# Performance work log

Measured on AMD Instinct MI355X. Metric: run time of the kernel, lower is better.

## Reference

```python
import jax, jax.numpy as jnp
import numpy as np

B, S, D, H, K = 8, 4096, 1024, 16, 256
DH = D // H  # attention_head_size = 64


def setup_inputs() -> dict:
    key = jax.random.key(0)
    ks = jax.random.split(key, 12)
    hidden_states = jax.random.normal(ks[0], (B, S, D), dtype=jnp.float32)
    # ragged lengths in [S/2, S]; HF-style additive mask: 0 valid, -10000 pad
    lengths = jax.random.randint(ks[1], (B,), S // 2, S + 1)
    attention_mask = jnp.where(
        jnp.arange(S)[None, :] < lengths[:, None], 0.0, -10000.0
    ).astype(jnp.float32)[:, None, None, :]  # [B,1,1,S]
    std = 0.02
    Wq = jax.random.normal(ks[2], (D, D), dtype=jnp.float32) * std
    bq = jnp.zeros((D,), dtype=jnp.float32)
    Wk = jax.random.normal(ks[3], (D, D), dtype=jnp.float32) * std
    bk = jnp.zeros((D,), dtype=jnp.float32)
    Wv = jax.random.normal(ks[4], (D, D), dtype=jnp.float32) * std
    bv = jnp.zeros((D,), dtype=jnp.float32)
    # nn.init.normal_(std=1.0), shape [max_position_embeddings, k]
    proj_k = jax.random.normal(ks[5], (S, K), dtype=jnp.float32)
    proj_v = jax.random.normal(ks[6], (S, K), dtype=jnp.float32)
    return dict(hidden_states=hidden_states, attention_mask=attention_mask,
                Wq=Wq, bq=bq, Wk=Wk, bk=bk, Wv=Wv, bv=bv,
                proj_k=proj_k, proj_v=proj_v)


def reference(hidden_states, attention_mask, Wq, bq, Wk, bk, Wv, bv, proj_k, proj_v):
    Bn, Sn, Dn = hidden_states.shape
    dt = hidden_states.dtype
    # lengths[i] = number of valid tokens (mask entries > -1)
    lengths = jnp.sum(attention_mask[:, 0, 0, :] > -1, axis=-1)  # [B] int
    m = (jnp.arange(Sn)[None, :] < lengths[:, None]).astype(dt)  # [B,S] valid mask
    pk = proj_k[:Sn]  # [S,K]
    pv = proj_v[:Sn]
    hk = hidden_states @ Wk.T + bk  # [B,S,D]
    hv = hidden_states @ Wv.T + bv
    # ragged projection: per sample, proj[:L_i]^T @ h[i,:L_i] / sqrt(L_i)
    # vectorized as a masked contraction (zeros beyond L_i contribute nothing)
    inv_sqrt_len = 1.0 / jnp.sqrt(lengths.astype(dt))  # [B]
    hkp = jnp.einsum('bs,sk,bsd->bkd', m, pk, hk) * inv_sqrt_len[:, None, None]
    hvp = jnp.einsum('bs,sk,bsd->bkd', m, pv, hv) * inv_sqrt_len[:, None, None]
    # split heads: [B,*,H,DH] -> [B,H,*,DH]
    q = (hidden_states @ Wq.T + bq).reshape(Bn, Sn, H, DH).transpose(0, 2, 1, 3)
    k = hkp.reshape(Bn, K, H, DH).transpose(0, 2, 1, 3)
    v = hvp.reshape(Bn, K, H, DH).transpose(0, 2, 1, 3)
    scores = jnp.einsum('bhsd,bhkd->bhsk', q, k) / np.float32(np.sqrt(DH))
    probs = jax.nn.softmax(scores, axis=-1)  # dropout p=0 (eval) -> identity
    ctx = jnp.einsum('bhsk,bhkd->bhsd', probs, v)
    return ctx.transpose(0, 2, 1, 3).reshape(Bn, Sn, Dn)
```

## Files before the change

kernel.cpp:

```cpp
#include <hip/hip_runtime.h>
#include <stdint.h>

#define B_ 8
#define S_ 4096
#define D_ 1024
#define H_ 16
#define K_ 256
#define DH_ 64

typedef unsigned short ushort_t;
typedef __attribute__((ext_vector_type(8))) short short8;
typedef __attribute__((ext_vector_type(4))) short short4x;
typedef __attribute__((ext_vector_type(4))) float floatx4;

static __device__ __forceinline__ float u2f(unsigned short u){
  union { float f; unsigned int i; } v; v.i = ((unsigned int)u) << 16; return v.f;
}
static __device__ __forceinline__ unsigned short f2u(float f){
  union { float f; unsigned int i; } v; v.f = f;
  unsigned int r = v.i + 0x7fffu + ((v.i >> 16) & 1u);
  return (unsigned short)(r >> 16);
}

__global__ __launch_bounds__(256) void k_len(const float* __restrict__ mask,
                                             int* __restrict__ len, float* __restrict__ invl){
  int b = blockIdx.x, t = threadIdx.x;
  __shared__ int cnt[256];
  int c = 0;
  for(int s = t; s < S_; s += 256) c += (mask[b*S_ + s] > -1.0f) ? 1 : 0;
  cnt[t] = c; __syncthreads();
  for(int o = 128; o > 0; o >>= 1){ if(t < o) cnt[t] += cnt[t+o]; __syncthreads(); }
  if(t == 0){ len[b] = cnt[0]; invl[b] = rsqrtf((float)cnt[0]); }
}

__global__ __launch_bounds__(256) void k_sp_part(const float* __restrict__ pk, const float* __restrict__ pv,
                                                 const float* __restrict__ mask, float* __restrict__ part){
  int c = blockIdx.x;
  int b = blockIdx.y;
  int sel = blockIdx.z;
  const float* p = sel ? pv : pk;
  int k = threadIdx.x;
  int s0 = c * 128;
  float acc = 0.f;
  for(int i = 0; i < 128; i++){
    int s = s0 + i;
    float mm = mask[b*S_ + s];
    if(mm > -1.0f) acc += p[(size_t)s*K_ + k];
  }
  part[(((size_t)(b*2 + sel))*32 + c)*K_ + k] = acc;
}

__global__ __launch_bounds__(256) void k_sp_red(const float* __restrict__ part, const float* __restrict__ invl,
                                                float* __restrict__ spk, float* __restrict__ spv){
  int b = blockIdx.x, sel = blockIdx.y, k = threadIdx.x;
  float acc = 0.f;
#pragma unroll
  for(int c = 0; c < 32; c++) acc += part[(((size_t)(b*2 + sel))*32 + c)*K_ + k];
  float r = acc * invl[b];
  if(sel) spv[b*K_ + k] = r; else spk[b*K_ + k] = r;
}

__global__ __launch_bounds__(256) void k_cvt(const float* __restrict__ src, ushort_t* __restrict__ dst, int n4){
  int i = blockIdx.x * 256 + threadIdx.x;
  if(i >= n4) return;
  const float4 a = *(const float4*)(src + i*4);
  short4x v;
  v[0] = (short)f2u(a.x); v[1] = (short)f2u(a.y); v[2] = (short)f2u(a.z); v[3] = (short)f2u(a.w);
  *(short4x*)(dst + i*4) = v;
}

__global__ __launch_bounds__(256) void k_trcvt(const float* __restrict__ src, ushort_t* __restrict__ dst,
                                               int R, int C, long sstride, long dstride){
  __shared__ __align__(16) short t[64*66];
  const float* s0 = src + (size_t)blockIdx.z * sstride;
  ushort_t* d0 = dst + (size_t)blockIdx.z * dstride;
  int r0 = blockIdx.y * 64, c0 = blockIdx.x * 64;
  int tid = threadIdx.x;
#pragma unroll
  for(int i = 0; i < 2; i++){
    int f = tid + 256*i;
    int r = f >> 3, c = (f & 7) * 8;
    const float* p = s0 + (size_t)(r0 + r) * C + (c0 + c);
    float4 a = *(const float4*)p;
    float4 b2 = *(const float4*)(p + 4);
    short* q = &t[r*66 + c];
    q[0]=(short)f2u(a.x); q[1]=(short)f2u(a.y); q[2]=(short)f2u(a.z); q[3]=(short)f2u(a.w);
    q[4]=(short)f2u(b2.x); q[5]=(short)f2u(b2.y); q[6]=(short)f2u(b2.z); q[7]=(short)f2u(b2.w);
  }
  __syncthreads();
#pragma unroll
  for(int i = 0; i < 2; i++){
    int f = tid + 256*i;
    int dc = f >> 3, sg = f & 7;
    short8 v;
#pragma unroll
    for(int j = 0; j < 8; j++) v[j] = t[(sg*8 + j)*66 + dc];
    *(short8*)(d0 + (size_t)(c0 + dc) * R + (r0 + sg*8)) = v;
  }
}

__global__ __launch_bounds__(256) void k_xp(const ushort_t* __restrict__ pkT, const ushort_t* __restrict__ pvT,
      const ushort_t* __restrict__ XT, const int* __restrict__ len, const float* __restrict__ invl,
      ushort_t* __restrict__ XpK, ushort_t* __restrict__ XpV){
  int b = blockIdx.y, sel = blockIdx.z;
  const ushort_t* A = sel ? pvT : pkT;
  ushort_t* hi = sel ? XpV : XpK;
  int m0 = (blockIdx.x & 1) * 128;
  int n0 = (blockIdx.x >> 1) * 128;
  const ushort_t* Bm = XT + (size_t)b * D_ * S_;
  int L = len[b];
  int nk = (L + 31) >> 5;
  bool tail = (L & 31) != 0;
  __shared__ __align__(16) short As[128*32];
  __shared__ __align__(16) short Bs[128*32];
  int tid = threadIdx.x, lane = tid & 63, w = tid >> 6;
  int mW = (w & 1) * 64, nW = (w >> 1) * 64;
  int lm = lane & 15, lk = (lane >> 4) * 8;
  floatx4 acc[4][4];
#pragma unroll
  for(int i = 0; i < 4; i++)
#pragma unroll
    for(int j = 0; j < 4; j++) acc[i][j] = (floatx4)0.f;
  for(int ks = 0; ks < nk; ks++){
    int k0 = ks << 5;
    short8 va[2], vb[2];
#pragma unroll
    for(int i = 0; i < 2; i++){
      int f = i*256 + tid;
      int row = f >> 2, col = (f & 3) * 8;
      va[i] = *(const short8*)(A  + (size_t)(m0+row)*S_ + (k0+col));
      vb[i] = *(const short8*)(Bm + (size_t)(n0+row)*S_ + (k0+col));
    }
    if(tail && ks == nk-1){
      int rlim = L - k0;
#pragma unroll
      for(int i = 0; i < 2; i++){
        int col = ((i*256 + tid) & 3) * 8;
#pragma unroll
        for(int j = 0; j < 8; j++) if(col + j >= rlim) va[i][j] = 0;
      }
    }
    __syncthreads();
#pragma unroll
    for(int i = 0; i < 2; i++){
      int f = i*256 + tid;
      *(short8*)&As[f*8] = va[i];
      *(short8*)&Bs[f*8] = vb[i];
    }
    __syncthreads();
    short8 af[4], bfr[4];
#pragma unroll
    for(int i = 0; i < 4; i++) af[i]  = *(const short8*)&As[(mW + 16*i + lm)*32 + lk];
#pragma unroll
    for(int j = 0; j < 4; j++) bfr[j] = *(const short8*)&Bs[(nW + 16*j + lm)*32 + lk];
#pragma unroll
    for(int i = 0; i < 4; i++)
#pragma unroll
      for(int j = 0; j < 4; j++)
        acc[i][j] = __builtin_amdgcn_mfma_f32_16x16x32_bf16(af[i], bfr[j], acc[i][j], 0, 0, 0);
  }
  float sc = invl[b];
#pragma unroll
  for(int i = 0; i < 4; i++){
#pragma unroll
    for(int j = 0; j < 4; j++){
      int col = n0 + nW + 16*j + lm;
#pragma unroll
      for(int r = 0; r < 4; r++){
        int row = m0 + mW + 16*i + (lane>>4)*4 + r;
        hi[((size_t)b*K_ + row)*D_ + col] = f2u(acc[i][j][r] * sc);
      }
    }
  }
}

__global__ __launch_bounds__(256) void k_kv(const ushort_t* __restrict__ XpK, const ushort_t* __restrict__ XpV,
      const ushort_t* __restrict__ Wk, const ushort_t* __restrict__ Wv,
      const float* __restrict__ bk, const float* __restrict__ bv,
      const float* __restrict__ spk, const float* __restrict__ spv,
      ushort_t* __restrict__ kten, ushort_t* __restrict__ vTt){
  int b = blockIdx.y, sel = blockIdx.z;
  const ushort_t* Ab = (sel ? XpV : XpK) + (size_t)b*K_*D_;
  const ushort_t* W = sel ? Wv : Wk;
  const float* bias = sel ? bv : bk;
  const float* sp = (sel ? spv : spk) + b*K_;
  int m0 = (blockIdx.x & 1) * 128;
  int n0 = (blockIdx.x >> 1) * 128;
  __shared__ __align__(16) short As[128*32];
  __shared__ __align__(16) short Bs[128*32];
  int tid = threadIdx.x, lane = tid & 63, w = tid >> 6;
  int mW = (w & 1) * 64, nW = (w >> 1) * 64;
  int lm = lane & 15, lk = (lane >> 4) * 8;
  floatx4 acc[4][4];
#pragma unroll
  for(int i = 0; i < 4; i++)
#pragma unroll
    for(int j = 0; j < 4; j++) acc[i][j] = (floatx4)0.f;
  for(int ks = 0; ks < 32; ks++){
    int k0 = ks << 5;
    short8 va[2], vb[2];
#pragma unroll
    for(int i = 0; i < 2; i++){
      int f = i*256 + tid;
      int row = f >> 2, col = (f & 3) * 8;
      va[i] = *(const short8*)(Ab + (size_t)(m0+row)*D_ + (k0+col));
      vb[i] = *(const short8*)(W  + (size_t)(n0+row)*D_ + (k0+col));
    }
    __syncthreads();
#pragma unroll
    for(int i = 0; i < 2; i++){
      int f = i*256 + tid;
      *(short8*)&As[f*8] = va[i];
      *(short8*)&Bs[f*8] = vb[i];
    }
    __syncthreads();
    short8 af[4], bfr[4];
#pragma unroll
    for(int i = 0; i < 4; i++) af[i]  = *(const short8*)&As[(mW + 16*i + lm)*32 + lk];
#pragma unroll
    for(int j = 0; j < 4; j++) bfr[j] = *(const short8*)&Bs[(nW + 16*j + lm)*32 + lk];
#pragma unroll
    for(int i = 0; i < 4; i++)
#pragma unroll
      for(int j = 0; j < 4; j++)
        acc[i][j] = __builtin_amdgcn_mfma_f32_16x16x32_bf16(af[i], bfr[j], acc[i][j], 0, 0, 0);
  }
#pragma unroll
  for(int j = 0; j < 4; j++){
    int col = n0 + nW + 16*j + lm;
    float bb = bias[col];
    int hcol = col >> 6, dcol = col & 63;
#pragma unroll
    for(int i = 0; i < 4; i++){
#pragma unroll
      for(int r = 0; r < 4; r++){
        int row = m0 + mW + 16*i + (lane>>4)*4 + r;
        float val = acc[i][j][r] + sp[row]*bb;
        if(sel == 0) kten[(((size_t)b*H_ + hcol)*K_ + row)*DH_ + dcol] = f2u(val);
        else         vTt [(((size_t)b*H_ + hcol)*DH_ + dcol)*K_ + row] = f2u(val);
      }
    }
  }
}

__global__ __launch_bounds__(256) void k_q(const float* __restrict__ X, const ushort_t* __restrict__ Wq,
                                           const float* __restrict__ bq, float* __restrict__ out){
  int m0 = (int)(blockIdx.x >> 3) * 128;
  int n0 = (int)(blockIdx.x & 7) * 128;
  __shared__ __align__(16) short As[128*32];
  __shared__ __align__(16) short Bs[128*32];
  int tid = threadIdx.x, lane = tid & 63, w = tid >> 6;
  int mW = (w & 1) * 64, nW = (w >> 1) * 64;
  int lm = lane & 15, lk = (lane >> 4) * 8;
  floatx4 acc[4][4];
#pragma unroll
  for(int i = 0; i < 4; i++)
#pragma unroll
    for(int j = 0; j < 4; j++) acc[i][j] = (floatx4)0.f;
  for(int ks = 0; ks < 32; ks++){
    int k0 = ks << 5;
    short8 va[2], vb[2];
#pragma unroll
    for(int i = 0; i < 2; i++){
      int f = i*256 + tid;
      int row = f >> 2, col = (f & 3) * 8;
      const float* p = X + (size_t)(m0+row)*D_ + (k0+col);
      float4 a = *(const float4*)p;
      float4 b2 = *(const float4*)(p + 4);
      short8 v;
      v[0]=(short)f2u(a.x); v[1]=(short)f2u(a.y); v[2]=(short)f2u(a.z); v[3]=(short)f2u(a.w);
      v[4]=(short)f2u(b2.x); v[5]=(short)f2u(b2.y); v[6]=(short)f2u(b2.z); v[7]=(short)f2u(b2.w);
      va[i] = v;
      vb[i] = *(const short8*)(Wq + (size_t)(n0+row)*D_ + (k0+col));
    }
    __syncthreads();
#pragma unroll
    for(int i = 0; i < 2; i++){
      int f = i*256 + tid;
      *(short8*)&As[f*8] = va[i];
      *(short8*)&Bs[f*8] = vb[i];
    }
    __syncthreads();
    short8 af[4], bfr[4];
#pragma unroll
    for(int i = 0; i < 4; i++) af[i]  = *(const short8*)&As[(mW + 16*i + lm)*32 + lk];
#pragma unroll
    for(int j = 0; j < 4; j++) bfr[j] = *(const short8*)&Bs[(nW + 16*j + lm)*32 + lk];
#pragma unroll
    for(int i = 0; i < 4; i++)
#pragma unroll
      for(int j = 0; j < 4; j++)
        acc[i][j] = __builtin_amdgcn_mfma_f32_16x16x32_bf16(af[i], bfr[j], acc[i][j], 0, 0, 0);
  }
#pragma unroll
  for(int j = 0; j < 4; j++){
    int col = n0 + nW + 16*j + lm;
    float bb = bq[col];
#pragma unroll
    for(int i = 0; i < 4; i++){
#pragma unroll
      for(int r = 0; r < 4; r++){
        int row = m0 + mW + 16*i + (lane>>4)*4 + r;
        out[(size_t)row*D_ + col] = acc[i][j][r] + bb;
      }
    }
  }
}

__global__ __launch_bounds__(256) void k_attn(float* __restrict__ out,
                                              const ushort_t* __restrict__ kten,
                                              const ushort_t* __restrict__ vTt){
  int x = blockIdx.x;
  int h = x & 15, b = (x >> 4) & 7, st = x >> 7;
  int s0 = st * 64;
  __shared__ __align__(16) short q_s[8*64*8];
  __shared__ __align__(16) short kp_s[8*256*8];
  __shared__ __align__(16) short v_s[32*64*8];
  int tid = threadIdx.x, lane = tid & 63, w = tid >> 6;
  int lm = lane & 15, lq = lane >> 4;
  const ushort_t* kb_g = kten + ((size_t)b*H_ + h)*K_*DH_;
  const ushort_t* vb_g = vTt + ((size_t)b*H_ + h)*DH_*K_;
  const float* qb_g = out + ((size_t)b*S_ + s0)*D_ + h*DH_;
  short8 vq[2], vk[8], vv[8];
#pragma unroll
  for(int i = 0; i < 2; i++){
    int f = i*256 + tid;
    const float* p = qb_g + (size_t)(f & 63)*D_ + (f >> 6)*8;
    float4 a = *(const float4*)p;
    float4 b2 = *(const float4*)(p + 4);
    short8 v;
    v[0]=(short)f2u(a.x); v[1]=(short)f2u(a.y); v[2]=(short)f2u(a.z); v[3]=(short)f2u(a.w);
    v[4]=(short)f2u(b2.x); v[5]=(short)f2u(b2.y); v[6]=(short)f2u(b2.z); v[7]=(short)f2u(b2.w);
    vq[i] = v;
  }
#pragma unroll
  for(int i = 0; i < 8; i++){
    int f = i*256 + tid;
    vk[i] = *(const short8*)(kb_g + (f & 255)*DH_ + (f >> 8)*8);
  }
#pragma unroll
  for(int i = 0; i < 8; i++){
    int f = i*256 + tid;
    vv[i] = *(const short8*)(vb_g + (f & 63)*K_ + (f >> 6)*8);
  }
#pragma unroll
  for(int i = 0; i < 2; i++) *(short8*)&q_s[(i*256 + tid)*8] = vq[i];
#pragma unroll
  for(int i = 0; i < 8; i++) *(short8*)&kp_s[(i*256 + tid)*8] = vk[i];
#pragma unroll
  for(int i = 0; i < 8; i++) *(short8*)&v_s[(i*256 + tid)*8] = vv[i];
  __syncthreads();

  int rw = w * 16;
  floatx4 accS[16];
#pragma unroll
  for(int n = 0; n < 16; n++) accS[n] = (floatx4)0.f;
#pragma unroll
  for(int ks = 0; ks < 2; ks++){
    int kb = ks*4 + lq;
    short8 a = *(const short8*)&q_s[(kb*64 + rw + lm)*8];
#pragma unroll
    for(int n = 0; n < 16; n++){
      short8 bf_ = *(const short8*)&kp_s[(kb*256 + 16*n + lm)*8];
      accS[n] = __builtin_amdgcn_mfma_f32_16x16x32_bf16(a, bf_, accS[n], 0, 0, 0);
    }
  }
  const float scl = 0.125f;
  float invr[4];
#pragma unroll
  for(int r = 0; r < 4; r++){
    float mx = -1e30f;
#pragma unroll
    for(int n = 0; n < 16; n++) mx = fmaxf(mx, accS[n][r]);
    mx = fmaxf(mx, __shfl_xor(mx, 1));
    mx = fmaxf(mx, __shfl_xor(mx, 2));
    mx = fmaxf(mx, __shfl_xor(mx, 4));
    mx = fmaxf(mx, __shfl_xor(mx, 8));
    float sum = 0.f;
#pragma unroll
    for(int n = 0; n < 16; n++){
      float p = __expf((accS[n][r] - mx) * scl);
      accS[n][r] = p;
      sum += p;
    }
    sum += __shfl_xor(sum, 1);
    sum += __shfl_xor(sum, 2);
    sum += __shfl_xor(sum, 4);
    sum += __shfl_xor(sum, 8);
    invr[r] = 1.f / sum;
  }
  __syncthreads();
  short* p_s = &kp_s[w * 4096];
#pragma unroll
  for(int n = 0; n < 16; n++){
    int kb2 = 2*n + (lm >> 3);
    int e = lane & 7;
#pragma unroll
    for(int r = 0; r < 4; r++){
      int row = lq*4 + r;
      p_s[(kb2*16 + row)*8 + e] = (short)f2u(accS[n][r]);
    }
  }
  floatx4 accC[4];
#pragma unroll
  for(int n = 0; n < 4; n++) accC[n] = (floatx4)0.f;
#pragma unroll
  for(int ks = 0; ks < 8; ks++){
    int kb = ks*4 + lq;
    short8 a = *(const short8*)&p_s[(kb*16 + lm)*8];
#pragma unroll
    for(int n = 0; n < 4; n++){
      short8 bf_ = *(const short8*)&v_s[(kb*64 + 16*n + lm)*8];
      accC[n] = __builtin_amdgcn_mfma_f32_16x16x32_bf16(a, bf_, accC[n], 0, 0, 0);
    }
  }
#pragma unroll
  for(int n = 0; n < 4; n++){
#pragma unroll
    for(int r = 0; r < 4; r++){
      int srow = s0 + rw + lq*4 + r;
      out[((size_t)b*S_ + srow)*D_ + h*DH_ + 16*n + lm] = accC[n][r] * invr[r];
    }
  }
}

extern "C" void kernel_launch(void* const* d_in, const int* in_sizes, int n_in,
                              void* d_out, int out_size, void* d_ws, size_t ws_size,
                              hipStream_t stream) {
  (void)in_sizes; (void)n_in; (void)out_size; (void)ws_size;
  const float* X    = (const float*)d_in[0];
  const float* mask = (const float*)d_in[1];
  const float* Wq   = (const float*)d_in[2];
  const float* bq   = (const float*)d_in[3];
  const float* Wk   = (const float*)d_in[4];
  const float* bk   = (const float*)d_in[5];
  const float* Wv   = (const float*)d_in[6];
  const float* bv   = (const float*)d_in[7];
  const float* pk   = (const float*)d_in[8];
  const float* pv   = (const float*)d_in[9];
  float* out = (float*)d_out;

  char* wsp = (char*)d_ws;
  int*   len  = (int*)wsp;
  float* invl = (float*)(wsp + 64);
  float* spk  = (float*)(wsp + 256);
  float* spv  = (float*)(wsp + 256 + 8192);
  ushort_t* pkT  = (ushort_t*)(wsp + 32768);
  ushort_t* pvT  = pkT  + (size_t)K_*S_;
  ushort_t* Wqb  = pvT  + (size_t)K_*S_;
  ushort_t* Wkb  = Wqb  + (size_t)D_*D_;
  ushort_t* Wvb  = Wkb  + (size_t)D_*D_;
  ushort_t* XpK  = Wvb  + (size_t)D_*D_;
  ushort_t* XpV  = XpK  + (size_t)B_*K_*D_;
  ushort_t* kten = XpV  + (size_t)B_*K_*D_;
  ushort_t* vTt  = kten + (size_t)B_*K_*D_;
  float* part = (float*)((char*)d_out + 100u*1024*1024);

  hipLaunchKernelGGL(k_len, dim3(8), dim3(256), 0, stream, mask, len, invl);
  hipLaunchKernelGGL(k_sp_part, dim3(32,8,2), dim3(256), 0, stream, pk, pv, mask, part);
  hipLaunchKernelGGL(k_sp_red,  dim3(8,2), dim3(256), 0, stream, part, invl, spk, spv);
  hipLaunchKernelGGL(k_cvt, dim3(1024), dim3(256), 0, stream, Wq, Wqb, D_*D_/4);
  hipLaunchKernelGGL(k_cvt, dim3(1024), dim3(256), 0, stream, Wk, Wkb, D_*D_/4);
  hipLaunchKernelGGL(k_cvt, dim3(1024), dim3(256), 0, stream, Wv, Wvb, D_*D_/4);
  hipLaunchKernelGGL(k_trcvt, dim3(4,64,1), dim3(256), 0, stream, pk, pkT, S_, K_, 0L, 0L);
  hipLaunchKernelGGL(k_trcvt, dim3(4,64,1), dim3(256), 0, stream, pv, pvT, S_, K_, 0L, 0L);
  hipLaunchKernelGGL(k_trcvt, dim3(16,64,8), dim3(256), 0, stream, X, (ushort_t*)out, S_, D_, (long)S_*D_, (long)D_*S_);
  hipLaunchKernelGGL(k_xp,  dim3(16,8,2), dim3(256), 0, stream, pkT, pvT, (const ushort_t*)out, len, invl, XpK, XpV);
  hipLaunchKernelGGL(k_kv,  dim3(16,8,2), dim3(256), 0, stream, XpK, XpV, Wkb, Wvb, bk, bv, spk, spv, kten, vTt);
  hipLaunchKernelGGL(k_q,   dim3(2048), dim3(256), 0, stream, X, Wqb, bq, out);
  hipLaunchKernelGGL(k_attn, dim3(8192), dim3(256), 0, stream, out, kten, vTt);
}
```

Before: 705.9 us.

## Emit bf16 copy of X alongside transpose; run Q GEMM and attention on bf16

The transpose-convert kernel now also writes a row-major bf16 copy of X into workspace. A new Q GEMM reads this bf16 X instead of converting fp32 on the fly, and it writes Q as bf16 to a workspace buffer rather than fp32 into the output. The attention kernel then loads bf16 Q, which halves Q traffic. The new path runs only when the workspace is large enough, so it needs about 128MB of extra scratch and falls back to the old path otherwise.

Measured after the change: 680.6 us. -3.6%, faster.

```diff
diff --git a/kernel.cpp b/kernel.cpp
--- a/kernel.cpp
+++ b/kernel.cpp
@@ -35,9 +35,7 @@
 
 __global__ __launch_bounds__(256) void k_sp_part(const float* __restrict__ pk, const float* __restrict__ pv,
                                                  const float* __restrict__ mask, float* __restrict__ part){
-  int c = blockIdx.x;
-  int b = blockIdx.y;
-  int sel = blockIdx.z;
+  int c = blockIdx.x, b = blockIdx.y, sel = blockIdx.z;
   const float* p = sel ? pv : pk;
   int k = threadIdx.x;
   int s0 = c * 128;
@@ -96,6 +94,44 @@
 #pragma unroll
     for(int j = 0; j < 8; j++) v[j] = t[(sg*8 + j)*66 + dc];
     *(short8*)(d0 + (size_t)(c0 + dc) * R + (r0 + sg*8)) = v;
+  }
+}
+
+__global__ __launch_bounds__(256) void k_trcvt_dual(const float* __restrict__ src, ushort_t* __restrict__ dstT,
+                                                    ushort_t* __restrict__ dstS, int R, int C,
+                                                    long sstride, long dTstride, long dSstride){
+  __shared__ __align__(16) short t[64*66];
+  const float* s0 = src + (size_t)blockIdx.z * sstride;
+  ushort_t* dT = dstT + (size_t)blockIdx.z * dTstride;
+  ushort_t* dS = dstS + (size_t)blockIdx.z * dSstride;
+  int r0 = blockIdx.y * 64, c0 = blockIdx.x * 64;
+  int tid = threadIdx.x;
+#pragma unroll
+  for(int i = 0; i < 2; i++){
+    int f = tid + 256*i;
+    int r = f >> 3, c = (f & 7) * 8;
+    const float* p = s0 + (size_t)(r0 + r) * C + (c0 + c);
+    float4 a = *(const float4*)p;
+    float4 b2 = *(const float4*)(p + 4);
+    short8 v;
+    v[0]=(short)f2u(a.x); v[1]=(short)f2u(a.y); v[2]=(short)f2u(a.z); v[3]=(short)f2u(a.w);
+    v[4]=(short)f2u(b2.x); v[5]=(short)f2u(b2.y); v[6]=(short)f2u(b2.z); v[7]=(short)f2u(b2.w);
+    *(short8*)(dS + (size_t)(r0 + r) * C + (c0 + c)) = v;
+    short* q = &t[r*66 + c];
+    const int* v32 = (const int*)&v;
+    int* q32 = (int*)q;
+#pragma unroll
+    for(int k2 = 0; k2 < 4; k2++) q32[k2] = v32[k2];
+  }
+  __syncthreads();
+#pragma unroll
+  for(int i = 0; i < 2; i++){
+    int f = tid + 256*i;
+    int dc = f >> 3, sg = f & 7;
+    short8 v;
+#pragma unroll
+    for(int j = 0; j < 8; j++) v[j] = t[(sg*8 + j)*66 + dc];
+    *(short8*)(dT + (size_t)(c0 + dc) * R + (r0 + sg*8)) = v;
   }
 }
 
@@ -307,6 +343,64 @@
   }
 }
 
+__global__ __launch_bounds__(256) void k_q2(const ushort_t* __restrict__ Xb, const ushort_t* __restrict__ Wq,
+                                            const float* __restrict__ bq, ushort_t* __restrict__ qb){
+  int m0 = (int)(blockIdx.x >> 3) * 128;
+  int n0 = (int)(blockIdx.x & 7) * 128;
+  __shared__ __align__(16) short As[128*32];
+  __shared__ __align__(16) short Bs[128*32];
+  int tid = threadIdx.x, lane = tid & 63, w = tid >> 6;
+  int mW = (w & 1) * 64, nW = (w >> 1) * 64;
+  int lm = lane & 15, lk = (lane >> 4) * 8;
+  floatx4 acc[4][4];
+#pragma unroll
+  for(int i = 0; i < 4; i++)
+#pragma unroll
+    for(int j = 0; j < 4; j++) acc[i][j] = (floatx4)0.f;
+  for(int ks = 0; ks < 32; ks++){
+    int k0 = ks << 5;
+    short8 va[2], vb[2];
+#pragma unroll
+    for(int i = 0; i < 2; i++){
+      int f = i*256 + tid;
+      int row = f >> 2, col = (f & 3) * 8;
+      va[i] = *(const short8*)(Xb + (size_t)(m0+row)*D_ + (k0+col));
+      vb[i] = *(const short8*)(Wq + (size_t)(n0+row)*D_ + (k0+col));
+    }
+    __syncthreads();
+#pragma unroll
+    for(int i = 0; i < 2; i++){
+      int f = i*256 + tid;
+      *(short8*)&As[f*8] = va[i];
+      *(short8*)&Bs[f*8] = vb[i];
+    }
+    __syncthreads();
+    short8 af[4], bfr[4];
+#pragma unroll
+    for(int i = 0; i < 4; i++) af[i]  = *(const short8*)&As[(mW + 16*i + lm)*32 + lk];
+#pragma unroll
+    for(int j = 0; j < 4; j++) bfr[j] = *(const short8*)&Bs[(nW + 16*j + lm)*32 + lk];
+#pragma unroll
+    for(int i = 0; i < 4; i++)
+#pragma unroll
+      for(int j = 0; j < 4; j++)
+        acc[i][j] = __builtin_amdgcn_mfma_f32_16x16x32_bf16(af[i], bfr[j], acc[i][j], 0, 0, 0);
+  }
+#pragma unroll
+  for(int j = 0; j < 4; j++){
+    int col = n0 + nW + 16*j + lm;
+    float bb = bq[col];
+#pragma unroll
+    for(int i = 0; i < 4; i++){
+#pragma unroll
+      for(int r = 0; r < 4; r++){
+        int row = m0 + mW + 16*i + (lane>>4)*4 + r;
+        qb[(size_t)row*D_ + col] = f2u(acc[i][j][r] + bb);
+      }
+    }
+  }
+}
+
 __global__ __launch_bounds__(256) void k_attn(float* __restrict__ out,
                                               const ushort_t* __restrict__ kten,
                                               const ushort_t* __restrict__ vTt){
@@ -424,10 +518,121 @@
   }
 }
 
+__global__ __launch_bounds__(256) void k_attn2(float* __restrict__ out, const ushort_t* __restrict__ qb,
+                                               const ushort_t* __restrict__ kten,
+                                               const ushort_t* __restrict__ vTt){
+  int x = blockIdx.x;
+  int h = x & 15, b = (x >> 4) & 7, st = x >> 7;
+  int s0 = st * 64;
+  __shared__ __align__(16) short q_s[8*64*8];
+  __shared__ __align__(16) short kp_s[8*256*8];
+  __shared__ __align__(16) short v_s[32*64*8];
+  int tid = threadIdx.x, lane = tid & 63, w = tid >> 6;
+  int lm = lane & 15, lq = lane >> 4;
+  const ushort_t* kb_g = kten + ((size_t)b*H_ + h)*K_*DH_;
+  const ushort_t* vb_g = vTt + ((size_t)b*H_ + h)*DH_*K_;
+  const ushort_t* qg = qb + ((size_t)b*S_ + s0)*D_ + h*DH_;
+  short8 vq[2], vk[8], vv[8];
+#pragma unroll
+  for(int i = 0; i < 2; i++){
+    int f = i*256 + tid;
+    vq[i] = *(const short8*)(qg + (size_t)(f & 63)*D_ + (f >> 6)*8);
+  }
+#pragma unroll
+  for(int i = 0; i < 8; i++){
+    int f = i*256 + tid;
+    vk[i] = *(const short8*)(kb_g + (f & 255)*DH_ + (f >> 8)*8);
+  }
+#pragma unroll
+  for(int i = 0; i < 8; i++){
+    int f = i*256 + tid;
+    vv[i] = *(const short8*)(vb_g + (f & 63)*K_ + (f >> 6)*8);
+  }
+#pragma unroll
+  for(int i = 0; i < 2; i++) *(short8*)&q_s[(i*256 + tid)*8] = vq[i];
+#pragma unroll
+  for(int i = 0; i < 8; i++) *(short8*)&kp_s[(i*256 + tid)*8] = vk[i];
+#pragma unroll
+  for(int i = 0; i < 8; i++) *(short8*)&v_s[(i*256 + tid)*8] = vv[i];
+  __syncthreads();
+
+  int rw = w * 16;
+  floatx4 accS[16];
+#pragma unroll
+  for(int n = 0; n < 16; n++) accS[n] = (floatx4)0.f;
+#pragma unroll
+  for(int ks = 0; ks < 2; ks++){
+    int kb = ks*4 + lq;
+    short8 a = *(const short8*)&q_s[(kb*64 + rw + lm)*8];
+#pragma unroll
+    for(int n = 0; n < 16; n++){
+      short8 bf_ = *(const short8*)&kp_s[(kb*256 + 16*n + lm)*8];
+      accS[n] = __builtin_amdgcn_mfma_f32_16x16x32_bf16(a, bf_, accS[n], 0, 0, 0);
+    }
+  }
+  const float scl = 0.125f;
+  float invr[4];
+#pragma unroll
+  for(int r = 0; r < 4; r++){
+    float mx = -1e30f;
+#pragma unroll
+    for(int n = 0; n < 16; n++) mx = fmaxf(mx, accS[n][r]);
+    mx = fmaxf(mx, __shfl_xor(mx, 1));
+    mx = fmaxf(mx, __shfl_xor(mx, 2));
+    mx = fmaxf(mx, __shfl_xor(mx, 4));
+    mx = fmaxf(mx, __shfl_xor(mx, 8));
+    float sum = 0.f;
+#pragma unroll
+    for(int n = 0; n < 16; n++){
+      float p = __expf((accS[n][r] - mx) * scl);
+      accS[n][r] = p;
+      sum += p;
+    }
+    sum += __shfl_xor(sum, 1);
+    sum += __shfl_xor(sum, 2);
+    sum += __shfl_xor(sum, 4);
+    sum += __shfl_xor(sum, 8);
+    invr[r] = 1.f / sum;
+  }
+  __syncthreads();
+  short* p_s = &kp_s[w * 4096];
+#pragma unroll
+  for(int n = 0; n < 16; n++){
+    int kb2 = 2*n + (lm >> 3);
+    int e = lane & 7;
+#pragma unroll
+    for(int r = 0; r < 4; r++){
+      int row = lq*4 + r;
+      p_s[(kb2*16 + row)*8 + e] = (short)f2u(accS[n][r]);
+    }
+  }
+  floatx4 accC[4];
+#pragma unroll
+  for(int n = 0; n < 4; n++) accC[n] = (floatx4)0.f;
+#pragma unroll
+  for(int ks = 0; ks < 8; ks++){
+    int kb = ks*4 + lq;
+    short8 a = *(const short8*)&p_s[(kb*16 + lm)*8];
+#pragma unroll
+    for(int n = 0; n < 4; n++){
+      short8 bf_ = *(const short8*)&v_s[(kb*64 + 16*n + lm)*8];
+      accC[n] = __builtin_amdgcn_mfma_f32_16x16x32_bf16(a, bf_, accC[n], 0, 0, 0);
+    }
+  }
+#pragma unroll
+  for(int n = 0; n < 4; n++){
+#pragma unroll
+    for(int r = 0; r < 4; r++){
+      int srow = s0 + rw + lq*4 + r;
+      out[((size_t)b*S_ + srow)*D_ + h*DH_ + 16*n + lm] = accC[n][r] * invr[r];
+    }
+  }
+}
+
 extern "C" void kernel_launch(void* const* d_in, const int* in_sizes, int n_in,
                               void* d_out, int out_size, void* d_ws, size_t ws_size,
                               hipStream_t stream) {
-  (void)in_sizes; (void)n_in; (void)out_size; (void)ws_size;
+  (void)in_sizes; (void)n_in; (void)out_size;
   const float* X    = (const float*)d_in[0];
   const float* mask = (const float*)d_in[1];
   const float* Wq   = (const float*)d_in[2];
@@ -454,6 +659,10 @@
   ushort_t* XpV  = XpK  + (size_t)B_*K_*D_;
   ushort_t* kten = XpV  + (size_t)B_*K_*D_;
   ushort_t* vTt  = kten + (size_t)B_*K_*D_;
+  ushort_t* Xb   = vTt  + (size_t)B_*K_*D_;
+  ushort_t* qb   = Xb   + (size_t)B_*S_*D_;
+  size_t tier2_need = (size_t)((char*)(qb + (size_t)B_*S_*D_) - wsp);
+  int tier2 = ws_size >= tier2_need;
   float* part = (float*)((char*)d_out + 100u*1024*1024);
 
   hipLaunchKernelGGL(k_len, dim3(8), dim3(256), 0, stream, mask, len, invl);
@@ -464,9 +673,18 @@
   hipLaunchKernelGGL(k_cvt, dim3(1024), dim3(256), 0, stream, Wv, Wvb, D_*D_/4);
   hipLaunchKernelGGL(k_trcvt, dim3(4,64,1), dim3(256), 0, stream, pk, pkT, S_, K_, 0L, 0L);
   hipLaunchKernelGGL(k_trcvt, dim3(4,64,1), dim3(256), 0, stream, pv, pvT, S_, K_, 0L, 0L);
-  hipLaunchKernelGGL(k_trcvt, dim3(16,64,8), dim3(256), 0, stream, X, (ushort_t*)out, S_, D_, (long)S_*D_, (long)D_*S_);
-  hipLaunchKernelGGL(k_xp,  dim3(16,8,2), dim3(256), 0, stream, pkT, pvT, (const ushort_t*)out, len, invl, XpK, XpV);
-  hipLaunchKernelGGL(k_kv,  dim3(16,8,2), dim3(256), 0, stream, XpK, XpV, Wkb, Wvb, bk, bv, spk, spv, kten, vTt);
-  hipLaunchKernelGGL(k_q,   dim3(2048), dim3(256), 0, stream, X, Wqb, bq, out);
-  hipLaunchKernelGGL(k_attn, dim3(8192), dim3(256), 0, stream, out, kten, vTt);
-}
+  if(tier2){
+    hipLaunchKernelGGL(k_trcvt_dual, dim3(16,64,8), dim3(256), 0, stream, X, (ushort_t*)out, Xb,
+                       S_, D_, (long)S_*D_, (long)D_*S_, (long)S_*D_);
+    hipLaunchKernelGGL(k_xp,  dim3(16,8,2), dim3(256), 0, stream, pkT, pvT, (const ushort_t*)out, len, invl, XpK, XpV);
+    hipLaunchKernelGGL(k_kv,  dim3(16,8,2), dim3(256), 0, stream, XpK, XpV, Wkb, Wvb, bk, bv, spk, spv, kten, vTt);
+    hipLaunchKernelGGL(k_q2,  dim3(2048), dim3(256), 0, stream, Xb, Wqb, bq, qb);
+    hipLaunchKernelGGL(k_attn2, dim3(8192), dim3(256), 0, stream, out, qb, kten, vTt);
+  } else {
+    hipLaunchKernelGGL(k_trcvt, dim3(16,64,8), dim3(256), 0, stream, X, (ushort_t*)out, S_, D_, (long)S_*D_, (long)D_*S_);
+    hipLaunchKernelGGL(k_xp,  dim3(16,8,2), dim3(256), 0, stream, pkT, pvT, (const ushort_t*)out, len, invl, XpK, XpV);
+    hipLaunchKernelGGL(k_kv,  dim3(16,8,2), dim3(256), 0, stream, XpK, XpV, Wkb, Wvb, bk, bv, spk, spv, kten, vTt);
+    hipLaunchKernelGGL(k_q,   dim3(2048), dim3(256), 0, stream, X, Wqb, bq, out);
+    hipLaunchKernelGGL(k_attn, dim3(8192), dim3(256), 0, stream, out, kten, vTt);
+  }
+}
```
